# Kernel tuning notes

Hardware: AMD Instinct MI355X
Metric: run time of the kernel (lower is better)

Reference implementation:

```python
import jax, jax.numpy as jnp
import numpy as np

NUM_BUCKETS = 32
MAX_DISTANCE = 128
NUM_HEADS = 16
D_KV = 64


def _relative_position_bucket(relative_position):
    # bidirectional buckets, faithful to T5Attention._relative_position_bucket
    num_buckets = NUM_BUCKETS // 2
    relative_buckets = (relative_position > 0).astype(jnp.int32) * num_buckets
    relative_position = jnp.abs(relative_position)
    max_exact = num_buckets // 2
    is_small = relative_position < max_exact
    rp_f = relative_position.astype(jnp.float32)
    rel_if_large = max_exact + (
        jnp.log(rp_f / max_exact) / np.log(MAX_DISTANCE / max_exact) * (num_buckets - max_exact)
    )
    rel_if_large = jnp.minimum(rel_if_large, num_buckets - 1)
    relative_buckets = relative_buckets + jnp.where(is_small, rp_f, rel_if_large).astype(jnp.int32)
    return relative_buckets


def setup_inputs() -> dict:
    key = jax.random.key(0)
    ks = jax.random.split(key, 6)
    B, S, D = 2, 2048, 1024
    inner = NUM_HEADS * D_KV  # 1024
    q_std = (inner * D_KV) ** (-0.5)
    kv_std = inner ** (-0.5)
    return {
        "hidden_states": jax.random.normal(ks[0], (B, S, D), jnp.float32),
        "attention_mask": jnp.ones((B, S), jnp.int32),
        "Wq": jax.random.normal(ks[1], (D, inner), jnp.float32) * q_std,
        "Wk": jax.random.normal(ks[2], (D, inner), jnp.float32) * kv_std,
        "Wv": jax.random.normal(ks[3], (D, inner), jnp.float32) * kv_std,
        "Wo": jax.random.normal(ks[4], (inner, D), jnp.float32) * kv_std,
        "rel_bias": jax.random.normal(ks[5], (NUM_BUCKETS, NUM_HEADS), jnp.float32),
    }


def reference(hidden_states, attention_mask, Wq, Wk, Wv, Wo, rel_bias):
    B, S, D = hidden_states.shape
    H, Dk = NUM_HEADS, D_KV

    q = (hidden_states @ Wq).reshape(B, S, H, Dk)
    k = (hidden_states @ Wk).reshape(B, S, H, Dk)
    v = (hidden_states @ Wv).reshape(B, S, H, Dk)
    q = q / jnp.sqrt(jnp.asarray(Dk, q.dtype))

    scores = jnp.einsum('bthd,bshd->bhts', q, k)  # [B,H,S,S]

    # relative position bias
    pos = jnp.arange(S, dtype=jnp.int32)
    rel_pos = pos[None, :] - pos[:, None]          # memory - context, [S,S]
    buckets = _relative_position_bucket(rel_pos)   # [S,S]
    bias = rel_bias[buckets]                       # [S,S,H]
    scores = scores + bias.transpose(2, 0, 1)[None].astype(scores.dtype)

    mask = attention_mask[:, None, None, :].astype(scores.dtype)
    scores = scores + (1.0 - mask) * jnp.finfo(scores.dtype).min

    attn = jax.nn.softmax(scores, axis=-1)
    out = jnp.einsum('bhts,bshd->bthd', attn, v).reshape(B, S, H * Dk)
    return out @ Wo
```

## Files before the change

### kernel.cpp

```cpp
#include <hip/hip_runtime.h>
#include <hip/hip_bf16.h>
#include <math.h>

typedef __attribute__((ext_vector_type(8))) short bf16x8;
typedef __attribute__((ext_vector_type(4))) short s16x4;
typedef __attribute__((ext_vector_type(4))) float f32x4;

constexpr int cB = 2, cS = 2048, cH = 16, cD = 64, cIn = 1024, cM = 1024;
constexpr float cLog2e = 1.4426950408889634f;

union BfPack { bf16x8 v; short s[8]; };
union BfPack4 { s16x4 v; short s[4]; };

__device__ __forceinline__ short f2bf(float f) {
    union { float f; unsigned u; } v; v.f = f;
    unsigned r = v.u + 0x7fffu + ((v.u >> 16) & 1u);
    return (short)(r >> 16);
}

__device__ __forceinline__ f32x4 mfma16(bf16x8 a, bf16x8 b, f32x4 c) {
    return __builtin_amdgcn_mfma_f32_16x16x32_bf16(a, b, c, 0, 0, 0);
}

__device__ __forceinline__ void async16(const short* g, short* l) {
    __builtin_amdgcn_global_load_lds(
        (const __attribute__((address_space(1))) unsigned*)(uintptr_t)g,
        (__attribute__((address_space(3))) unsigned*)(uintptr_t)l, 16, 0, 0);
}

__global__ __launch_bounds__(256) void prep_kernel(
    const float* __restrict__ hidden, short* __restrict__ hbf,
    const float* __restrict__ Wq, const float* __restrict__ Wk,
    const float* __restrict__ Wv, const float* __restrict__ Wo,
    short* __restrict__ Wt,
    const float* __restrict__ rel_bias, const int* __restrict__ mask,
    float* __restrict__ bt, float* __restrict__ maskadd) {
    const int bid = blockIdx.x;
    const int tid = threadIdx.x;
    if (bid < 2048) {
        int t = bid * 256 + tid;
        const float4* src = (const float4*)hidden;
        float4 a = src[2 * t], b = src[2 * t + 1];
        BfPack p;
        p.s[0] = f2bf(a.x); p.s[1] = f2bf(a.y); p.s[2] = f2bf(a.z); p.s[3] = f2bf(a.w);
        p.s[4] = f2bf(b.x); p.s[5] = f2bf(b.y); p.s[6] = f2bf(b.z); p.s[7] = f2bf(b.w);
        ((bf16x8*)hbf)[t] = p.v;
    } else if (bid < 3072) {
        const int b2 = bid - 2048;
        const int z = b2 >> 8, rem = b2 & 255;
        const float* W = (z == 0) ? Wq : (z == 1) ? Wk : (z == 2) ? Wv : Wo;
        const float scale = (z == 0) ? 0.125f * cLog2e : 1.0f;
        const int n0 = (rem & 15) * 64, k0 = (rem >> 4) * 64;
        __shared__ short sW[64][72];
        const int r = tid >> 2, c4 = (tid & 3) * 16;
        {
            const float* src = W + (size_t)(k0 + r) * cM + n0 + c4;
            BfPack p[2];
            #pragma unroll
            for (int q = 0; q < 2; q++) {
                float4 x = ((const float4*)src)[2 * q];
                float4 y = ((const float4*)src)[2 * q + 1];
                p[q].s[0] = f2bf(x.x * scale); p[q].s[1] = f2bf(x.y * scale);
                p[q].s[2] = f2bf(x.z * scale); p[q].s[3] = f2bf(x.w * scale);
                p[q].s[4] = f2bf(y.x * scale); p[q].s[5] = f2bf(y.y * scale);
                p[q].s[6] = f2bf(y.z * scale); p[q].s[7] = f2bf(y.w * scale);
            }
            *(bf16x8*)&sW[r][c4] = p[0].v;
            *(bf16x8*)&sW[r][c4 + 8] = p[1].v;
        }
        __syncthreads();
        const int n = tid >> 2, kc = (tid & 3) * 16;
        BfPack o0, o1;
        #pragma unroll
        for (int j = 0; j < 8; j++) o0.s[j] = sW[kc + j][n];
        #pragma unroll
        for (int j = 0; j < 8; j++) o1.s[j] = sW[kc + 8 + j][n];
        short* dst = Wt + (size_t)z * cM * cIn + (size_t)(n0 + n) * cIn + k0 + kc;
        *(bf16x8*)dst = o0.v;
        *(bf16x8*)(dst + 8) = o1.v;
    } else {
        int idx = (bid - 3072) * 256 + tid;
        if (idx < 4096) maskadd[idx] = (1.0f - (float)mask[idx]) * -3.0e38f;
        if (idx >= 4095) return;
        int delta = idx - 2047;
        int rb = (delta > 0) ? 16 : 0;
        int ar = delta < 0 ? -delta : delta;
        int bucket;
        if (ar < 8) {
            bucket = rb + ar;
        } else {
            float rl = 8.0f + logf((float)ar * 0.125f) * 2.8853900817779268f;
            rl = fminf(rl, 15.0f);
            bucket = rb + (int)rl;
        }
        #pragma unroll
        for (int h = 0; h < cH; h++)
            bt[h * 4096 + 2048 + delta] = rel_bias[bucket * cH + h] * cLog2e;
    }
}

template <bool SWAP>
__device__ __forceinline__ void gemm_core(
    const short* __restrict__ A, const short* __restrict__ Bt,
    short* smem, int m0, int c0, int tid, f32x4 (&acc)[4][4]) {
    const int w = tid >> 6, l = tid & 63;
    const int m16 = l & 15, g = l >> 4;
    const int srow = l >> 2, scol = (l & 3) * 8;
    const int mq = (w & 1) * 64, nq = (w >> 1) * 64;

    const short* pA0 = A + (size_t)(m0 + w * 16 + srow) * cIn + scol;
    const short* pA1 = A + (size_t)(m0 + 64 + w * 16 + srow) * cIn + scol;
    const short* pB0 = Bt + (size_t)(c0 + w * 16 + srow) * cIn + scol;
    const short* pB1 = Bt + (size_t)(c0 + 64 + w * 16 + srow) * cIn + scol;
    const int dof = w * 512 + l * 8;

    async16(pA0, smem + dof);
    async16(pA1, smem + 2048 + dof);
    async16(pB0, smem + 4096 + dof);
    async16(pB1, smem + 6144 + dof);
    __syncthreads();

    for (int k0 = 0; k0 < cIn; k0 += 32) {
        const int buf = (k0 >> 5) & 1;
        if (k0 + 32 < cIn) {
            short* dn = smem + (buf ^ 1) * 8192 + dof;
            async16(pA0 + k0 + 32, dn);
            async16(pA1 + k0 + 32, dn + 2048);
            async16(pB0 + k0 + 32, dn + 4096);
            async16(pB1 + k0 + 32, dn + 6144);
        }
        const short* sA = smem + buf * 8192;
        const short* sB = sA + 4096;
        bf16x8 af[4], bf[4];
        #pragma unroll
        for (int i = 0; i < 4; i++)
            af[i] = *(const bf16x8*)(sA + (mq + i * 16 + m16) * 32 + g * 8);
        #pragma unroll
        for (int j = 0; j < 4; j++)
            bf[j] = *(const bf16x8*)(sB + (nq + j * 16 + m16) * 32 + g * 8);
        #pragma unroll
        for (int i = 0; i < 4; i++)
            #pragma unroll
            for (int j = 0; j < 4; j++)
                acc[i][j] = SWAP ? mfma16(bf[j], af[i], acc[i][j])
                                 : mfma16(af[i], bf[j], acc[i][j]);
        __syncthreads();
    }
}

__global__ __launch_bounds__(256) void gemm_qkv_kernel(
    const short* __restrict__ hbf, const short* __restrict__ Wt,
    short* __restrict__ Qrm, short* __restrict__ Krm, short* __restrict__ VT) {
    const int raw = blockIdx.x;
    const int xcd = raw & 7;
    const int rest = raw >> 3;
    const int cblk = rest & 7;
    const int t = rest >> 3;
    const int z = t >> 2;
    const int m0 = (xcd * 4 + (t & 3)) * 128;
    const int c0 = cblk * 128;

    const short* Bt = Wt + (size_t)z * cM * cIn;
    __shared__ short smem[128 * 132];
    const int tid = threadIdx.x, w = tid >> 6, l = tid & 63;
    const int m16 = l & 15, g = l >> 4;
    const int mq = (w & 1) * 64, nq = (w >> 1) * 64;
    f32x4 acc[4][4] = {};

    if (z <= 1) {
        gemm_core<false>(hbf, Bt, smem, m0, c0, tid, acc);
        __syncthreads();
        #pragma unroll
        for (int i = 0; i < 4; i++)
            #pragma unroll
            for (int j = 0; j < 4; j++)
                #pragma unroll
                for (int r = 0; r < 4; r++)
                    smem[(mq + i * 16 + g * 4 + r) * 132 + nq + j * 16 + m16] =
                        f2bf(acc[i][j][r]);
        __syncthreads();
        const int tr = tid >> 1, hf = (tid & 1) * 64;
        short* dst = ((z == 0) ? Qrm : Krm) + (size_t)(m0 + tr) * cM + c0 + hf;
        #pragma unroll
        for (int c = 0; c < 8; c++)
            *(bf16x8*)(dst + c * 8) = *(const bf16x8*)(smem + tr * 132 + hf + c * 8);
    } else {
        gemm_core<true>(hbf, Bt, smem, m0, c0, tid, acc);
        __syncthreads();
        #pragma unroll
        for (int i = 0; i < 4; i++) {
            const int sl = mq + i * 16 + m16;
            const int s6 = sl & 63;
            const int pcol = (sl & 64) +
                             ((s6 & 3) | ((s6 & 28) << 1) | ((s6 >> 3) & 4));
            #pragma unroll
            for (int j = 0; j < 4; j++)
                #pragma unroll
                for (int r = 0; r < 4; r++)
                    smem[(nq + j * 16 + g * 4 + r) * 132 + pcol] =
                        f2bf(acc[i][j][r]);
        }
        __syncthreads();
        const int tr = tid >> 1, hf = (tid & 1) * 64;
        const int wcol = c0 + tr;
        short* dst = VT + (((size_t)(m0 >> 11) * cH + (wcol >> 6)) * cD +
                           (wcol & 63)) * cS + (m0 & 2047) + hf;
        #pragma unroll
        for (int c = 0; c < 8; c++)
            *(bf16x8*)(dst + c * 8) = *(const bf16x8*)(smem + tr * 132 + hf + c * 8);
    }
}

__global__ __launch_bounds__(512, 1) void attn_kernel(
    const short* __restrict__ Qrm, const short* __restrict__ Krm,
    const short* __restrict__ VTK, const float* __restrict__ maskadd,
    const float* __restrict__ bias_t, short* __restrict__ ctx) {
    const int raw = blockIdx.x;
    const int xcd = raw & 7, j = raw >> 3;
    const int qi = j & 7, grp = j >> 3;
    const int bh = grp * 8 + xcd;
    const int b = bh >> 4, h = bh & 15;
    const int q0 = qi * 256;

    const short* VTp = VTK + ((size_t)b * cH + h) * cS * cD;
    const float* mp = maskadd + b * cS;

    const int tid = threadIdx.x;
    const int wave = tid >> 6, lane = tid & 63;
    const int m16 = lane & 15, g = lane >> 4;

    __shared__ short Kt[2][128 * 64];
    __shared__ short Vt[2][64 * 128];
    __shared__ float bias_lds[2304];
    __shared__ float mask_lds[2048];

    {
        const float* bw = bias_t + h * 4096 + 2048 - (q0 + 255);
        for (int i = tid; i < 2303; i += 512)
            bias_lds[i] = bw[i];
        ((f32x4*)mask_lds)[tid & 511] = ((const f32x4*)mp)[tid & 511];
    }

    int qv[2];
    bf16x8 qf[2][2];
    #pragma unroll
    for (int qq = 0; qq < 2; qq++) {
        qv[qq] = q0 + wave * 16 + qq * 128 + m16;
        const short* qb = Qrm + (size_t)(b * cS + qv[qq]) * cM + h * cD;
        qf[qq][0] = *(const bf16x8*)(qb + g * 8);
        qf[qq][1] = *(const bf16x8*)(qb + 32 + g * 8);
    }

    int ib[2];
    #pragma unroll
    for (int qq = 0; qq < 2; qq++)
        ib[qq] = q0 + 255 + g * 4 - qv[qq];

    f32x4 o[2][4] = {};
    f32x4 lacc[2] = {};
    BfPack ones;
    #pragma unroll
    for (int i = 0; i < 8; i++) ones.s[i] = (short)0x3F80;

    const int u8 = tid & 7, r8 = tid >> 3;
    const int u16s = tid & 15, r16 = tid >> 4;
    const short* pK = Krm + ((size_t)b * cS + r8) * cM + h * cD +
                      ((u8 ^ (r8 & 7)) << 3);
    const short* pV = VTp + (size_t)r16 * cS + ((u16s ^ (r16 & 7)) << 3);
    short* dK = (short*)Kt + tid * 8;
    short* dV = (short*)Vt + tid * 8;

    const int kx0 = ((g ^ (m16 & 7)) << 3);
    const int kx1 = (((g + 4) ^ (m16 & 7)) << 3);

    #pragma unroll
    for (int c = 0; c < 2; c++) {
        async16(pK + (size_t)(c * 64) * cM, dK + c * 4096);
        async16(pV + (size_t)(c * 32) * cS, dV + c * 4096);
    }
    __syncthreads();

    for (int kt = 0; kt < cS; kt += 128) {
        const int buf = (kt >> 7) & 1, nxt = buf ^ 1;
        if (kt + 128 < cS) {
            #pragma unroll
            for (int c = 0; c < 2; c++) {
                async16(pK + (size_t)(kt + 128 + c * 64) * cM,
                        dK + nxt * 8192 + c * 4096);
                async16(pV + (size_t)(c * 32) * cS + kt + 128,
                        dV + nxt * 8192 + c * 4096);
            }
        }
        const short* K_ = (const short*)Kt + buf * 8192;
        const short* V_ = (const short*)Vt + buf * 8192;
        const int iq0 = ib[0] + kt, iq1 = ib[1] + kt;

        #pragma unroll
        for (int h2 = 0; h2 < 2; h2++) {
            f32x4 binit[2][4];
            #pragma unroll
            for (int t4 = 0; t4 < 4; t4++) {
                const int sto = (h2 * 4 + t4) * 16;
                f32x4 mk = *(const f32x4*)(mask_lds + kt + sto + g * 4);
                #pragma unroll
                for (int c = 0; c < 4; c++) {
                    binit[0][t4][c] = bias_lds[iq0 + sto + c] + mk[c];
                    binit[1][t4][c] = bias_lds[iq1 + sto + c] + mk[c];
                }
            }

            f32x4 s[2][4];
            __builtin_amdgcn_s_setprio(1);
            #pragma unroll
            for (int t4 = 0; t4 < 4; t4++) {
                const int st = h2 * 4 + t4;
                bf16x8 klo = *(const bf16x8*)(K_ + (st * 16 + m16) * 64 + kx0);
                bf16x8 khi = *(const bf16x8*)(K_ + (st * 16 + m16) * 64 + kx1);
                #pragma unroll
                for (int qq = 0; qq < 2; qq++)
                    s[qq][t4] = mfma16(khi, qf[qq][1],
                                       mfma16(klo, qf[qq][0], binit[qq][t4]));
            }
            __builtin_amdgcn_s_setprio(0);

            BfPack pp[2][2];
            #pragma unroll
            for (int qq = 0; qq < 2; qq++)
                #pragma unroll
                for (int t4 = 0; t4 < 4; t4++)
                    #pragma unroll
                    for (int r = 0; r < 2; r++) {
                        float p0 = __builtin_amdgcn_exp2f(s[qq][t4][2 * r]);
                        float p1 = __builtin_amdgcn_exp2f(s[qq][t4][2 * r + 1]);
                        __hip_bfloat162 h2v = __float22bfloat162_rn(float2{p0, p1});
                        short2 sp = *(short2*)&h2v;
                        pp[qq][t4 & 1].s[(t4 >> 1) * 4 + 2 * r]     = sp.x;
                        pp[qq][t4 & 1].s[(t4 >> 1) * 4 + 2 * r + 1] = sp.y;
                    }

            __builtin_amdgcn_s_setprio(1);
            #pragma unroll
            for (int qq = 0; qq < 2; qq++) {
                lacc[qq] = mfma16(ones.v, pp[qq][0].v, lacc[qq]);
                lacc[qq] = mfma16(ones.v, pp[qq][1].v, lacc[qq]);
            }
            #pragma unroll
            for (int nt = 0; nt < 4; nt++) {
                bf16x8 vlo = *(const bf16x8*)(V_ + (nt * 16 + m16) * 128 +
                                              h2 * 64 + kx0);
                bf16x8 vhi = *(const bf16x8*)(V_ + (nt * 16 + m16) * 128 +
                                              h2 * 64 + kx1);
                #pragma unroll
                for (int qq = 0; qq < 2; qq++) {
                    o[qq][nt] = mfma16(vlo, pp[qq][0].v, o[qq][nt]);
                    o[qq][nt] = mfma16(vhi, pp[qq][1].v, o[qq][nt]);
                }
            }
            __builtin_amdgcn_s_setprio(0);
        }

        __syncthreads();
    }

    #pragma unroll
    for (int qq = 0; qq < 2; qq++) {
        const float inv = 1.0f / lacc[qq][0];
        short* cb = ctx + (size_t)(b * cS + qv[qq]) * cM + h * cD;
        #pragma unroll
        for (int nt = 0; nt < 4; nt++) {
            BfPack4 pk;
            #pragma unroll
            for (int r = 0; r < 4; r++) pk.s[r] = f2bf(o[qq][nt][r] * inv);
            *(s16x4*)(cb + nt * 16 + g * 4) = pk.v;
        }
    }
}

__global__ __launch_bounds__(256) void gemm_o_kernel(
    const short* __restrict__ ctx, const short* __restrict__ WoT,
    float* __restrict__ out) {
    const int raw = blockIdx.x;
    const int xcd = raw & 7;
    const int rest = raw >> 3;
    const int cblk = rest & 7;
    const int m0 = (xcd * 8 + (rest >> 3)) * 64;
    const int c0 = cblk * 128;

    __shared__ short smem[12288];
    const int tid = threadIdx.x, w = tid >> 6, l = tid & 63;
    const int m16 = l & 15, g = l >> 4;
    const int wm = (w & 1) * 32, wn = (w >> 1) * 64;
    const int sr = tid >> 2, sc = (tid & 3) * 8;
    f32x4 acc[2][4] = {};

    const short* pA = ctx + (size_t)(m0 + sr) * cIn + sc;
    const short* pB0 = WoT + (size_t)(c0 + sr) * cIn + sc;
    const short* pB1 = WoT + (size_t)(c0 + 64 + sr) * cIn + sc;

    async16(pA, smem + tid * 8);
    async16(pB0, smem + 2048 + tid * 8);
    async16(pB1, smem + 4096 + tid * 8);
    __syncthreads();

    for (int k0 = 0; k0 < cIn; k0 += 32) {
        const int buf = (k0 >> 5) & 1;
        if (k0 + 32 < cIn) {
            short* dn = smem + (buf ^ 1) * 6144 + tid * 8;
            async16(pA + k0 + 32, dn);
            async16(pB0 + k0 + 32, dn + 2048);
            async16(pB1 + k0 + 32, dn + 4096);
        }
        const short* sA = smem + buf * 6144;
        const short* sB = sA + 2048;
        bf16x8 af[2], bf[4];
        #pragma unroll
        for (int i = 0; i < 2; i++)
            af[i] = *(const bf16x8*)(sA + (wm + i * 16 + m16) * 32 + g * 8);
        #pragma unroll
        for (int jj = 0; jj < 4; jj++)
            bf[jj] = *(const bf16x8*)(sB + (wn + jj * 16 + m16) * 32 + g * 8);
        #pragma unroll
        for (int i = 0; i < 2; i++)
            #pragma unroll
            for (int jj = 0; jj < 4; jj++)
                acc[i][jj] = mfma16(af[i], bf[jj], acc[i][jj]);
        __syncthreads();
    }
    #pragma unroll
    for (int i = 0; i < 2; i++)
        #pragma unroll
        for (int jj = 0; jj < 4; jj++)
            #pragma unroll
            for (int r = 0; r < 4; r++)
                out[(size_t)(m0 + wm + i * 16 + g * 4 + r) * cM +
                    c0 + wn + jj * 16 + m16] = acc[i][jj][r];
}

extern "C" void kernel_launch(void* const* d_in, const int* in_sizes, int n_in,
                              void* d_out, int out_size, void* d_ws, size_t ws_size,
                              hipStream_t stream) {
    const float* hidden   = (const float*)d_in[0];
    const int*   mask     = (const int*)d_in[1];
    const float* Wq       = (const float*)d_in[2];
    const float* Wk       = (const float*)d_in[3];
    const float* Wv       = (const float*)d_in[4];
    const float* Wo       = (const float*)d_in[5];
    const float* rel_bias = (const float*)d_in[6];
    float* out = (float*)d_out;

    short* hbf_ctx = (short*)d_ws;
    short* Wt  = hbf_ctx + (size_t)4 * 1024 * 1024;
    short* Qrm = Wt  + (size_t)4 * 1024 * 1024;
    short* Krm = Qrm + (size_t)4 * 1024 * 1024;
    short* VT  = Krm + (size_t)4 * 1024 * 1024;
    float* bias_t  = (float*)(VT + (size_t)4 * 1024 * 1024);
    float* maskf   = bias_t + 16 * 4096;

    prep_kernel<<<3088, 256, 0, stream>>>(hidden, hbf_ctx, Wq, Wk, Wv, Wo, Wt,
                                          rel_bias, mask, bias_t, maskf);
    gemm_qkv_kernel<<<768, 256, 0, stream>>>(hbf_ctx, Wt, Qrm, Krm, VT);
    attn_kernel<<<256, 512, 0, stream>>>(Qrm, Krm, VT, maskf, bias_t, hbf_ctx);
    gemm_o_kernel<<<512, 256, 0, stream>>>(hbf_ctx, Wt + (size_t)3 * 1024 * 1024,
                                           out);
}
```

Measured before the change: 187.2 us.

## Load GEMM weight fragments directly into registers and remap blocks for XCD weight locality

In the QKV and output projection GEMMs, the weight (B) operand is now loaded from global memory straight into MFMA register fragments, double-buffered in registers. Only the activation (A) tile still goes through LDS. The k-loop is unrolled by two with explicit ping-pong buffers. Block-to-tile mapping changes so each XCD owns one column block of weights, which should improve L2 reuse of weights within an XCD. This cuts LDS traffic and footprint, but adds register pressure and uncoalesced per-lane 16-byte global loads for B, and it loses A-tile reuse locality across XCDs.

Measured after the change: 239.3 us. 27.9% more time.

```diff
diff --git a/kernel.cpp b/kernel.cpp
--- a/kernel.cpp
+++ b/kernel.cpp
@@ -110,41 +110,62 @@
 
     const short* pA0 = A + (size_t)(m0 + w * 16 + srow) * cIn + scol;
     const short* pA1 = A + (size_t)(m0 + 64 + w * 16 + srow) * cIn + scol;
-    const short* pB0 = Bt + (size_t)(c0 + w * 16 + srow) * cIn + scol;
-    const short* pB1 = Bt + (size_t)(c0 + 64 + w * 16 + srow) * cIn + scol;
     const int dof = w * 512 + l * 8;
+
+    const short* pB[4];
+    #pragma unroll
+    for (int j = 0; j < 4; j++)
+        pB[j] = Bt + (size_t)(c0 + nq + j * 16 + m16) * cIn + g * 8;
 
     async16(pA0, smem + dof);
     async16(pA1, smem + 2048 + dof);
-    async16(pB0, smem + 4096 + dof);
-    async16(pB1, smem + 6144 + dof);
+    bf16x8 bfA[4], bfB[4];
+    #pragma unroll
+    for (int j = 0; j < 4; j++) bfA[j] = *(const bf16x8*)pB[j];
     __syncthreads();
 
-    for (int k0 = 0; k0 < cIn; k0 += 32) {
-        const int buf = (k0 >> 5) & 1;
-        if (k0 + 32 < cIn) {
-            short* dn = smem + (buf ^ 1) * 8192 + dof;
-            async16(pA0 + k0 + 32, dn);
-            async16(pA1 + k0 + 32, dn + 2048);
-            async16(pB0 + k0 + 32, dn + 4096);
-            async16(pB1 + k0 + 32, dn + 6144);
-        }
-        const short* sA = smem + buf * 8192;
-        const short* sB = sA + 4096;
-        bf16x8 af[4], bf[4];
-        #pragma unroll
-        for (int i = 0; i < 4; i++)
-            af[i] = *(const bf16x8*)(sA + (mq + i * 16 + m16) * 32 + g * 8);
-        #pragma unroll
-        for (int j = 0; j < 4; j++)
-            bf[j] = *(const bf16x8*)(sB + (nq + j * 16 + m16) * 32 + g * 8);
-        #pragma unroll
-        for (int i = 0; i < 4; i++)
-            #pragma unroll
-            for (int j = 0; j < 4; j++)
-                acc[i][j] = SWAP ? mfma16(bf[j], af[i], acc[i][j])
-                                 : mfma16(af[i], bf[j], acc[i][j]);
-        __syncthreads();
+    for (int k0 = 0; k0 < cIn; k0 += 64) {
+        {
+            if (k0 + 32 < cIn) {
+                async16(pA0 + k0 + 32, smem + 4096 + dof);
+                async16(pA1 + k0 + 32, smem + 6144 + dof);
+                #pragma unroll
+                for (int j = 0; j < 4; j++)
+                    bfB[j] = *(const bf16x8*)(pB[j] + k0 + 32);
+            }
+            bf16x8 af[4];
+            #pragma unroll
+            for (int i = 0; i < 4; i++)
+                af[i] = *(const bf16x8*)(smem + (mq + i * 16 + m16) * 32 + g * 8);
+            #pragma unroll
+            for (int i = 0; i < 4; i++)
+                #pragma unroll
+                for (int j = 0; j < 4; j++)
+                    acc[i][j] = SWAP ? mfma16(bfA[j], af[i], acc[i][j])
+                                     : mfma16(af[i], bfA[j], acc[i][j]);
+            __syncthreads();
+        }
+        {
+            if (k0 + 64 < cIn) {
+                async16(pA0 + k0 + 64, smem + dof);
+                async16(pA1 + k0 + 64, smem + 2048 + dof);
+                #pragma unroll
+                for (int j = 0; j < 4; j++)
+                    bfA[j] = *(const bf16x8*)(pB[j] + k0 + 64);
+            }
+            bf16x8 af[4];
+            #pragma unroll
+            for (int i = 0; i < 4; i++)
+                af[i] = *(const bf16x8*)(smem + 4096 +
+                                         (mq + i * 16 + m16) * 32 + g * 8);
+            #pragma unroll
+            for (int i = 0; i < 4; i++)
+                #pragma unroll
+                for (int j = 0; j < 4; j++)
+                    acc[i][j] = SWAP ? mfma16(bfB[j], af[i], acc[i][j])
+                                     : mfma16(af[i], bfB[j], acc[i][j]);
+            __syncthreads();
+        }
     }
 }
 
@@ -154,11 +175,10 @@
     const int raw = blockIdx.x;
     const int xcd = raw & 7;
     const int rest = raw >> 3;
-    const int cblk = rest & 7;
-    const int t = rest >> 3;
-    const int z = t >> 2;
-    const int m0 = (xcd * 4 + (t & 3)) * 128;
-    const int c0 = cblk * 128;
+    const int mblk = rest & 31;
+    const int z = rest >> 5;
+    const int m0 = mblk * 128;
+    const int c0 = xcd * 128;
 
     const short* Bt = Wt + (size_t)z * cM * cIn;
     __shared__ short smem[128 * 132];
@@ -382,11 +402,10 @@
     const int raw = blockIdx.x;
     const int xcd = raw & 7;
     const int rest = raw >> 3;
-    const int cblk = rest & 7;
-    const int m0 = (xcd * 8 + (rest >> 3)) * 64;
-    const int c0 = cblk * 128;
-
-    __shared__ short smem[12288];
+    const int m0 = rest * 64;
+    const int c0 = xcd * 128;
+
+    __shared__ short smem[4096];
     const int tid = threadIdx.x, w = tid >> 6, l = tid & 63;
     const int m16 = l & 15, g = l >> 4;
     const int wm = (w & 1) * 32, wn = (w >> 1) * 64;
@@ -394,37 +413,55 @@
     f32x4 acc[2][4] = {};
 
     const short* pA = ctx + (size_t)(m0 + sr) * cIn + sc;
-    const short* pB0 = WoT + (size_t)(c0 + sr) * cIn + sc;
-    const short* pB1 = WoT + (size_t)(c0 + 64 + sr) * cIn + sc;
+    const short* pB[4];
+    #pragma unroll
+    for (int j = 0; j < 4; j++)
+        pB[j] = WoT + (size_t)(c0 + wn + j * 16 + m16) * cIn + g * 8;
 
     async16(pA, smem + tid * 8);
-    async16(pB0, smem + 2048 + tid * 8);
-    async16(pB1, smem + 4096 + tid * 8);
+    bf16x8 bfA[4], bfB[4];
+    #pragma unroll
+    for (int j = 0; j < 4; j++) bfA[j] = *(const bf16x8*)pB[j];
     __syncthreads();
 
-    for (int k0 = 0; k0 < cIn; k0 += 32) {
-        const int buf = (k0 >> 5) & 1;
-        if (k0 + 32 < cIn) {
-            short* dn = smem + (buf ^ 1) * 6144 + tid * 8;
-            async16(pA + k0 + 32, dn);
-            async16(pB0 + k0 + 32, dn + 2048);
-            async16(pB1 + k0 + 32, dn + 4096);
-        }
-        const short* sA = smem + buf * 6144;
-        const short* sB = sA + 2048;
-        bf16x8 af[2], bf[4];
-        #pragma unroll
-        for (int i = 0; i < 2; i++)
-            af[i] = *(const bf16x8*)(sA + (wm + i * 16 + m16) * 32 + g * 8);
-        #pragma unroll
-        for (int jj = 0; jj < 4; jj++)
-            bf[jj] = *(const bf16x8*)(sB + (wn + jj * 16 + m16) * 32 + g * 8);
-        #pragma unroll
-        for (int i = 0; i < 2; i++)
-            #pragma unroll
-            for (int jj = 0; jj < 4; jj++)
-                acc[i][jj] = mfma16(af[i], bf[jj], acc[i][jj]);
-        __syncthreads();
+    for (int k0 = 0; k0 < cIn; k0 += 64) {
+        {
+            if (k0 + 32 < cIn) {
+                async16(pA + k0 + 32, smem + 2048 + tid * 8);
+                #pragma unroll
+                for (int j = 0; j < 4; j++)
+                    bfB[j] = *(const bf16x8*)(pB[j] + k0 + 32);
+            }
+            bf16x8 af[2];
+            #pragma unroll
+            for (int i = 0; i < 2; i++)
+                af[i] = *(const bf16x8*)(smem + (wm + i * 16 + m16) * 32 + g * 8);
+            #pragma unroll
+            for (int i = 0; i < 2; i++)
+                #pragma unroll
+                for (int jj = 0; jj < 4; jj++)
+                    acc[i][jj] = mfma16(af[i], bfA[jj], acc[i][jj]);
+            __syncthreads();
+        }
+        {
+            if (k0 + 64 < cIn) {
+                async16(pA + k0 + 64, smem + tid * 8);
+                #pragma unroll
+                for (int j = 0; j < 4; j++)
+                    bfA[j] = *(const bf16x8*)(pB[j] + k0 + 64);
+            }
+            bf16x8 af[2];
+            #pragma unroll
+            for (int i = 0; i < 2; i++)
+                af[i] = *(const bf16x8*)(smem + 2048 +
+                                         (wm + i * 16 + m16) * 32 + g * 8);
+            #pragma unroll
+            for (int i = 0; i < 2; i++)
+                #pragma unroll
+                for (int jj = 0; jj < 4; jj++)
+                    acc[i][jj] = mfma16(af[i], bfB[jj], acc[i][jj]);
+            __syncthreads();
+        }
     }
     #pragma unroll
     for (int i = 0; i < 2; i++)
```

## Triple-buffer GEMM core with two-deep async prefetch and one barrier per step

Applied to the files above, without the earlier changes.

Changes the QKV GEMM main loop from double buffering with two syncthreads per iteration to a three-stage LDS ring. Two tiles are prefetched ahead, and the loop uses explicit vmcnt waits plus a single barrier per k-step. The goal is to hide global-load latency and cut synchronisation overhead. In exchange the shared allocation grows to 48KB, which may reduce occupancy. Other kernels that call gemm_core must also have at least 24576 shorts of smem.

After: 192.9 us. +3.1%, slower.

```diff
diff --git a/kernel.cpp b/kernel.cpp
--- a/kernel.cpp
+++ b/kernel.cpp
@@ -114,22 +114,33 @@
     const short* pB1 = Bt + (size_t)(c0 + 64 + w * 16 + srow) * cIn + scol;
     const int dof = w * 512 + l * 8;
 
-    async16(pA0, smem + dof);
-    async16(pA1, smem + 2048 + dof);
-    async16(pB0, smem + 4096 + dof);
-    async16(pB1, smem + 6144 + dof);
-    __syncthreads();
-
-    for (int k0 = 0; k0 < cIn; k0 += 32) {
-        const int buf = (k0 >> 5) & 1;
-        if (k0 + 32 < cIn) {
-            short* dn = smem + (buf ^ 1) * 8192 + dof;
-            async16(pA0 + k0 + 32, dn);
-            async16(pA1 + k0 + 32, dn + 2048);
-            async16(pB0 + k0 + 32, dn + 4096);
-            async16(pB1 + k0 + 32, dn + 6144);
-        }
-        const short* sA = smem + buf * 8192;
+    #pragma unroll
+    for (int t = 0; t < 2; t++) {
+        short* dn = smem + t * 8192 + dof;
+        async16(pA0 + t * 32, dn);
+        async16(pA1 + t * 32, dn + 2048);
+        async16(pB0 + t * 32, dn + 4096);
+        async16(pB1 + t * 32, dn + 6144);
+    }
+
+    for (int t = 0; t < 32; t++) {
+        if (t == 31)
+            asm volatile("s_waitcnt vmcnt(0)" ::: "memory");
+        else
+            asm volatile("s_waitcnt vmcnt(4)" ::: "memory");
+        __builtin_amdgcn_s_barrier();
+        __builtin_amdgcn_sched_barrier(0);
+
+        if (t + 2 < 32) {
+            const int k2 = (t + 2) * 32;
+            short* dn = smem + ((t + 2) % 3) * 8192 + dof;
+            async16(pA0 + k2, dn);
+            async16(pA1 + k2, dn + 2048);
+            async16(pB0 + k2, dn + 4096);
+            async16(pB1 + k2, dn + 6144);
+        }
+
+        const short* sA = smem + (t % 3) * 8192;
         const short* sB = sA + 4096;
         bf16x8 af[4], bf[4];
         #pragma unroll
@@ -144,7 +155,6 @@
             for (int j = 0; j < 4; j++)
                 acc[i][j] = SWAP ? mfma16(bf[j], af[i], acc[i][j])
                                  : mfma16(af[i], bf[j], acc[i][j]);
-        __syncthreads();
     }
 }
 
@@ -161,7 +171,7 @@
     const int c0 = cblk * 128;
 
     const short* Bt = Wt + (size_t)z * cM * cIn;
-    __shared__ short smem[128 * 132];
+    __shared__ short smem[24576];
     const int tid = threadIdx.x, w = tid >> 6, l = tid & 63;
     const int m16 = l & 15, g = l >> 4;
     const int mq = (w & 1) * 64, nq = (w >> 1) * 64;
```
